# Kernel tuning notes

Hardware: AMD Instinct MI355X
Metric: run time of the kernel (lower is better)

Reference implementation:

```python
import jax, jax.numpy as jnp
import numpy as np

B, IN, H, L = 128, 256, 1024, 256
nA, nB = H // 2, (H - 1) // 2        # pairs per A-layer / B-layer
LB = L // 2
LA = L - LB                           # A layers come first when L is odd
PI = float(np.pi)


def setup_inputs() -> dict:
    key = jax.random.key(0)
    ks = jax.random.split(key, 14)
    u = lambda k, shp: jax.random.uniform(k, shp, minval=-PI, maxval=PI)
    return {
        "inputsR": jax.random.normal(ks[0], (B, IN), dtype=jnp.float32),
        "inputsI": jax.random.normal(ks[1], (B, IN), dtype=jnp.float32),
        "stateR": jax.random.normal(ks[2], (B, H), dtype=jnp.float32),
        "stateI": jax.random.normal(ks[3], (B, H), dtype=jnp.float32),
        # CLinear params (init_scale=0.01 inside RNNCellCmplx)
        "weightR": 0.01 * jax.random.normal(ks[4], (H, IN), dtype=jnp.float32),
        "weightI": 0.01 * jax.random.normal(ks[5], (H, IN), dtype=jnp.float32),
        "biasR": 0.01 * jax.random.normal(ks[6], (H,), dtype=jnp.float32),
        "biasI": 0.01 * jax.random.normal(ks[7], (H,), dtype=jnp.float32),
        # Clements mesh angles, uniform(-pi, pi)
        "angleA0": u(ks[8], (LA, nA)),
        "angleA1": u(ks[9], (LA, nA)),
        "angleB0": u(ks[10], (LB, nB)),
        "angleB1": u(ks[11], (LB, nB)),
        # diagonal phase + modReLU bias (both init to zero)
        "omega": jnp.zeros((H,), dtype=jnp.float32),
        "mod_bias": jnp.zeros((H,), dtype=jnp.float32),
    }


def _mzi(ar, ai, br, bi, th0, th1):
    """PSDC MZI on channel pairs: phase shifter e^{i*th0} on arm a, then a
    directional coupler with coupling angle th1 (unitary 2x2)."""
    c0, s0 = jnp.cos(th0), jnp.sin(th0)
    pr = c0 * ar - s0 * ai          # p = e^{i th0} * a
    pi_ = s0 * ar + c0 * ai
    c, s = jnp.cos(th1), jnp.sin(th1)
    oar = c * pr - s * bi           # a' = cos*p + i sin*b
    oai = c * pi_ + s * br
    obr = c * br - s * pi_          # b' = i sin*p + cos*b
    obi = c * bi + s * pr
    return oar, oai, obr, obi


def _layerA(xr, xi, t0, t1):
    Bs, N = xr.shape
    oar, oai, obr, obi = _mzi(xr[:, 0::2], xi[:, 0::2], xr[:, 1::2], xi[:, 1::2], t0, t1)
    xr = jnp.stack([oar, obr], axis=-1).reshape(Bs, N)
    xi = jnp.stack([oai, obi], axis=-1).reshape(Bs, N)
    return xr, xi


def _layerB(xr, xi, t0, t1):
    Bs, N = xr.shape  # pairs (1,2),(3,4),... ; channels 0 and N-1 pass through
    oar, oai, obr, obi = _mzi(xr[:, 1:-1:2], xi[:, 1:-1:2], xr[:, 2::2], xi[:, 2::2], t0, t1)
    midr = jnp.stack([oar, obr], axis=-1).reshape(Bs, N - 2)
    midi = jnp.stack([oai, obi], axis=-1).reshape(Bs, N - 2)
    xr = jnp.concatenate([xr[:, :1], midr, xr[:, -1:]], axis=1)
    xi = jnp.concatenate([xi[:, :1], midi, xi[:, -1:]], axis=1)
    return xr, xi


def _clements(xr, xi, A0, A1, B0, B1):
    def step(carry, ang):
        cr, ci = carry
        a0, a1, b0, b1 = ang
        cr, ci = _layerA(cr, ci, a0, a1)
        cr, ci = _layerB(cr, ci, b0, b1)
        return (cr, ci), None
    (xr, xi), _ = jax.lax.scan(step, (xr, xi), (A0[:LB], A1[:LB], B0, B1))
    for k in range(LB, LA):  # trailing A layer when num_layers is odd (static)
        xr, xi = _layerA(xr, xi, A0[k], A1[k])
    return xr, xi


def _forward(inputsR, inputsI, stateR, stateI, weightR, weightI, biasR, biasI,
             angleA0, angleA1, angleB0, angleB1, omega, mod_bias):
    # CLinear: complex y = W x + b
    ihR = inputsR @ weightR.T - inputsI @ weightI.T + biasR
    ihI = inputsR @ weightI.T + inputsI @ weightR.T + biasI
    # Clements unitary mesh on hidden state
    hr, hi = _clements(stateR, stateI, angleA0, angleA1, angleB0, angleB1)
    # diagonal phase e^{i omega}
    co, so = jnp.cos(omega), jnp.sin(omega)
    hhR = co * hr - so * hi
    hhI = so * hr + co * hi
    # complex add
    zr = ihR + hhR
    zi = ihI + hhI
    # modReLU: relu(|z| + b) * z / |z|
    mag = jnp.sqrt(zr * zr + zi * zi)
    scale = jax.nn.relu(mag + mod_bias) / jnp.maximum(mag, 1e-8)
    return jnp.stack([scale * zr, scale * zi])  # (2, B, H)


def reference(inputsR, inputsI, stateR, stateI, weightR, weightI, biasR, biasI,
              angleA0, angleA1, angleB0, angleB1, omega, mod_bias):
    return _forward(inputsR, inputsI, stateR, stateI, weightR, weightI, biasR, biasI,
                    angleA0, angleA1, angleB0, angleB1, omega, mod_bias)
```

## Files before the change

### kernel.cpp

```cpp
#include <hip/hip_runtime.h>
#include <math.h>

#define NBATCH 128
#define NIN    256
#define NH     1024
#define NSTEPS 128
#define NA     512
#define NB     511
#define NBP    512

#define TABA_OFF 0
#define TABB_OFF (NSTEPS * NBP * 4)
#define IHR_OFF  (TABB_OFF + NSTEPS * NBP * 4)
#define IHI_OFF  (IHR_OFF + NBATCH * NH)

__global__ __launch_bounds__(256) void trig_kernel(
    const float* __restrict__ A0, const float* __restrict__ A1,
    const float* __restrict__ B0, const float* __restrict__ B1,
    float* __restrict__ ws)
{
    int idx = blockIdx.x * blockDim.x + threadIdx.x;
    const int totalA = NSTEPS * NA;
    const int totalB = NSTEPS * NB;
    if (idx < totalA) {
        int l = idx >> 9;
        int p = idx & 511;
        float a0 = A0[idx], a1 = A1[idx];
        float4 v = make_float4(cosf(a0), sinf(a0), cosf(a1), sinf(a1));
        ((float4*)(ws + TABA_OFF))[l * NBP + p] = v;
    } else {
        int j = idx - totalA;
        if (j < totalB) {
            int l = j / NB;
            int p = j - l * NB;
            float b0 = B0[j], b1 = B1[j];
            float4 v = make_float4(cosf(b0), sinf(b0), cosf(b1), sinf(b1));
            ((float4*)(ws + TABB_OFF))[l * NBP + p] = v;
        }
    }
}

__global__ __launch_bounds__(256) void gemm_kernel(
    const float* __restrict__ inR, const float* __restrict__ inI,
    const float* __restrict__ wR,  const float* __restrict__ wI,
    const float* __restrict__ biasR, const float* __restrict__ biasI,
    float* __restrict__ ws)
{
    __shared__ float ldsR[16 * 260];
    __shared__ float ldsI[16 * 260];
    const int h0 = blockIdx.x * 16;
    const int b0 = blockIdx.y * 16;
    const int tid = threadIdx.x;

    for (int e = tid; e < 16 * 64; e += 256) {
        int bb = e >> 6;
        int k4 = e & 63;
        float4 vr = ((const float4*)(inR + (b0 + bb) * NIN))[k4];
        float4 vi = ((const float4*)(inI + (b0 + bb) * NIN))[k4];
        *(float4*)&ldsR[bb * 260 + k4 * 4] = vr;
        *(float4*)&ldsI[bb * 260 + k4 * 4] = vi;
    }
    __syncthreads();

    const int hl = tid & 15, bl = tid >> 4;
    const int h = h0 + hl, bb = b0 + bl;
    const float4* wr4 = (const float4*)(wR + h * NIN);
    const float4* wi4 = (const float4*)(wI + h * NIN);

    float accR = 0.f, accI = 0.f;
#pragma unroll 8
    for (int k4 = 0; k4 < 64; ++k4) {
        float4 wr = wr4[k4];
        float4 wi = wi4[k4];
        float4 xr = *(const float4*)&ldsR[bl * 260 + k4 * 4];
        float4 xi = *(const float4*)&ldsI[bl * 260 + k4 * 4];
        accR += xr.x * wr.x - xi.x * wi.x;
        accI += xr.x * wi.x + xi.x * wr.x;
        accR += xr.y * wr.y - xi.y * wi.y;
        accI += xr.y * wi.y + xi.y * wr.y;
        accR += xr.z * wr.z - xi.z * wi.z;
        accI += xr.z * wi.z + xi.z * wr.z;
        accR += xr.w * wr.w - xi.w * wi.w;
        accI += xr.w * wi.w + xi.w * wr.w;
    }
    float* ihR = ws + IHR_OFF;
    float* ihI = ws + IHI_OFF;
    ihR[bb * NH + h] = accR + biasR[h];
    ihI[bb * NH + h] = accI + biasI[h];
}

__global__ __launch_bounds__(256) void mesh_kernel(
    const float* __restrict__ stateR, const float* __restrict__ stateI,
    const float* __restrict__ omega,  const float* __restrict__ mod_bias,
    const float* __restrict__ ws, float* __restrict__ out)
{
    __shared__ float xch[2][2][256][2];

    const int b = blockIdx.x;
    const int t = threadIdx.x;
    const float4* tA = (const float4*)(ws + TABA_OFF);
    const float4* tB = (const float4*)(ws + TABB_OFF);

    float4 sr = ((const float4*)(stateR + b * NH))[t];
    float4 si = ((const float4*)(stateI + b * NH))[t];
    float cr0 = sr.x, cr1 = sr.y, cr2 = sr.z, cr3 = sr.w;
    float ci0 = si.x, ci1 = si.y, ci2 = si.z, ci3 = si.w;

    float4 a0  = tA[2 * t];
    float4 a1  = tA[2 * t + 1];
    float4 b_l = tB[2 * t - 1];
    float4 b_c = tB[2 * t];
    float4 b_r = tB[2 * t + 1];

    for (int l = 0; l < NSTEPS; ++l) {
        const int ln = (l < NSTEPS - 1) ? (l + 1) : (NSTEPS - 1);
        float4 na0 = tA[ln * NBP + 2 * t];
        float4 na1 = tA[ln * NBP + 2 * t + 1];
        float4 nbl = tB[ln * NBP + 2 * t - 1];
        float4 nbc = tB[ln * NBP + 2 * t];
        float4 nbr = tB[ln * NBP + 2 * t + 1];

        {
            float pr = a0.x * cr0 - a0.y * ci0;
            float pi = a0.y * cr0 + a0.x * ci0;
            float tr = cr1, ti = ci1;
            cr0 = a0.z * pr - a0.w * ti;
            ci0 = a0.z * pi + a0.w * tr;
            cr1 = a0.z * tr - a0.w * pi;
            ci1 = a0.z * ti + a0.w * pr;
        }
        {
            float pr = a1.x * cr2 - a1.y * ci2;
            float pi = a1.y * cr2 + a1.x * ci2;
            float tr = cr3, ti = ci3;
            cr2 = a1.z * pr - a1.w * ti;
            ci2 = a1.z * pi + a1.w * tr;
            cr3 = a1.z * tr - a1.w * pi;
            ci3 = a1.z * ti + a1.w * pr;
        }

        const int buf = l & 1;
        xch[buf][0][t][0] = cr0; xch[buf][0][t][1] = ci0;
        xch[buf][1][t][0] = cr3; xch[buf][1][t][1] = ci3;
        __syncthreads();

        {
            float pr = b_c.x * cr1 - b_c.y * ci1;
            float pi = b_c.y * cr1 + b_c.x * ci1;
            float tr = cr2, ti = ci2;
            cr1 = b_c.z * pr - b_c.w * ti;
            ci1 = b_c.z * pi + b_c.w * tr;
            cr2 = b_c.z * tr - b_c.w * pi;
            ci2 = b_c.z * ti + b_c.w * pr;
        }
        if (t < 255) {
            float rr = xch[buf][0][t + 1][0];
            float ri = xch[buf][0][t + 1][1];
            float pr = b_r.x * cr3 - b_r.y * ci3;
            float pi = b_r.y * cr3 + b_r.x * ci3;
            cr3 = b_r.z * pr - b_r.w * ri;
            ci3 = b_r.z * pi + b_r.w * rr;
        }
        if (t > 0) {
            float lr = xch[buf][1][t - 1][0];
            float li = xch[buf][1][t - 1][1];
            float pr = b_l.x * lr - b_l.y * li;
            float pi = b_l.y * lr + b_l.x * li;
            float nr = b_l.z * cr0 - b_l.w * pi;
            float ni = b_l.z * ci0 + b_l.w * pr;
            cr0 = nr; ci0 = ni;
        }

        a0 = na0; a1 = na1; b_l = nbl; b_c = nbc; b_r = nbr;
    }

    float4 om = ((const float4*)omega)[t];
    float4 mb = ((const float4*)mod_bias)[t];
    float4 ir = ((const float4*)(ws + IHR_OFF + b * NH))[t];
    float4 ii = ((const float4*)(ws + IHI_OFF + b * NH))[t];

    float hr[4] = {cr0, cr1, cr2, cr3};
    float hi[4] = {ci0, ci1, ci2, ci3};
    float oms[4] = {om.x, om.y, om.z, om.w};
    float mbs[4] = {mb.x, mb.y, mb.z, mb.w};
    float irs[4] = {ir.x, ir.y, ir.z, ir.w};
    float iis[4] = {ii.x, ii.y, ii.z, ii.w};
    float orr[4], ori[4];
#pragma unroll
    for (int j = 0; j < 4; ++j) {
        float co = cosf(oms[j]);
        float so = sinf(oms[j]);
        float hhR = co * hr[j] - so * hi[j];
        float hhI = so * hr[j] + co * hi[j];
        float zr = irs[j] + hhR;
        float zi = iis[j] + hhI;
        float mag = sqrtf(zr * zr + zi * zi);
        float sc = fmaxf(mag + mbs[j], 0.f) / fmaxf(mag, 1e-8f);
        orr[j] = sc * zr;
        ori[j] = sc * zi;
    }
    float4 o0 = make_float4(orr[0], orr[1], orr[2], orr[3]);
    float4 o1 = make_float4(ori[0], ori[1], ori[2], ori[3]);
    ((float4*)(out + b * NH))[t] = o0;
    ((float4*)(out + NBATCH * NH + b * NH))[t] = o1;
}

extern "C" void kernel_launch(void* const* d_in, const int* in_sizes, int n_in,
                              void* d_out, int out_size, void* d_ws, size_t ws_size,
                              hipStream_t stream)
{
    const float* inputsR = (const float*)d_in[0];
    const float* inputsI = (const float*)d_in[1];
    const float* stateR  = (const float*)d_in[2];
    const float* stateI  = (const float*)d_in[3];
    const float* weightR = (const float*)d_in[4];
    const float* weightI = (const float*)d_in[5];
    const float* biasR   = (const float*)d_in[6];
    const float* biasI   = (const float*)d_in[7];
    const float* angleA0 = (const float*)d_in[8];
    const float* angleA1 = (const float*)d_in[9];
    const float* angleB0 = (const float*)d_in[10];
    const float* angleB1 = (const float*)d_in[11];
    const float* omega   = (const float*)d_in[12];
    const float* mod_b   = (const float*)d_in[13];
    float* ws = (float*)d_ws;
    float* out = (float*)d_out;

    {
        int total = NSTEPS * NA + NSTEPS * NB;
        int blocks = (total + 255) / 256;
        hipLaunchKernelGGL(trig_kernel, dim3(blocks), dim3(256), 0, stream,
                           angleA0, angleA1, angleB0, angleB1, ws);
    }
    hipLaunchKernelGGL(gemm_kernel, dim3(NH / 16, NBATCH / 16), dim3(256), 0,
                       stream, inputsR, inputsI, weightR, weightI,
                       biasR, biasI, ws);
    hipLaunchKernelGGL(mesh_kernel, dim3(NBATCH), dim3(256), 0, stream,
                       stateR, stateI, omega, mod_b, ws, out);
}
```

Before: 165.6 us.

## Run mesh in one wavefront per batch row with shuffles, merge prep kernels

The mesh kernel now uses a single 64-lane wavefront per batch row, with each lane holding 16 channels in registers. Neighbour exchange across lanes goes through wave shuffles, which removes the shared-memory exchange and the per-layer block barrier. The trig tables are re-laid out as lane-interleaved so each lane's loads coalesce, and the complex GEMM is retiled with LDS staging and merged with the trig precompute into one launch. Only 128 wavefronts run the serial mesh, so GPU occupancy is very low, and each lane does four times the arithmetic plus register pressure from prefetching 17 float4 values.

```diff
diff --git a/kernel.cpp b/kernel.cpp
--- a/kernel.cpp
+++ b/kernel.cpp
@@ -7,202 +7,229 @@
 #define NSTEPS 128
 #define NA     512
 #define NB     511
-#define NBP    512
 
 #define TABA_OFF 0
-#define TABB_OFF (NSTEPS * NBP * 4)
-#define IHR_OFF  (TABB_OFF + NSTEPS * NBP * 4)
+#define TABB_OFF (NSTEPS * 512 * 4)
+#define IHR_OFF  (TABB_OFF + NSTEPS * 512 * 4)
 #define IHI_OFF  (IHR_OFF + NBATCH * NH)
 
-__global__ __launch_bounds__(256) void trig_kernel(
+#define GEMM_BLOCKS 128
+#define PREP_BLOCKS (GEMM_BLOCKS + 512)
+
+__global__ __launch_bounds__(256) void prep_kernel(
+    const float* __restrict__ inR, const float* __restrict__ inI,
+    const float* __restrict__ wR,  const float* __restrict__ wI,
+    const float* __restrict__ biasR, const float* __restrict__ biasI,
     const float* __restrict__ A0, const float* __restrict__ A1,
     const float* __restrict__ B0, const float* __restrict__ B1,
     float* __restrict__ ws)
 {
-    int idx = blockIdx.x * blockDim.x + threadIdx.x;
-    const int totalA = NSTEPS * NA;
-    const int totalB = NSTEPS * NB;
-    if (idx < totalA) {
-        int l = idx >> 9;
-        int p = idx & 511;
-        float a0 = A0[idx], a1 = A1[idx];
-        float4 v = make_float4(cosf(a0), sinf(a0), cosf(a1), sinf(a1));
-        ((float4*)(ws + TABA_OFF))[l * NBP + p] = v;
-    } else {
-        int j = idx - totalA;
-        if (j < totalB) {
-            int l = j / NB;
-            int p = j - l * NB;
-            float b0 = B0[j], b1 = B1[j];
-            float4 v = make_float4(cosf(b0), sinf(b0), cosf(b1), sinf(b1));
-            ((float4*)(ws + TABB_OFF))[l * NBP + p] = v;
-        }
+    __shared__ float xr_s[64][68], xi_s[64][68];
+    __shared__ float wr_s[16][68], wi_s[16][68];
+
+    if (blockIdx.x >= GEMM_BLOCKS) {
+        int idx = (blockIdx.x - GEMM_BLOCKS) * 256 + threadIdx.x;
+        const int totalA = NSTEPS * NA;
+        const int totalB = NSTEPS * NB;
+        float4* tA = (float4*)(ws + TABA_OFF);
+        float4* tB = (float4*)(ws + TABB_OFF);
+        if (idx < totalA) {
+            int l = idx >> 9, p = idx & 511;
+            int lane = p >> 3, j = p & 7;
+            float a0 = A0[idx], a1 = A1[idx];
+            tA[l * 512 + j * 64 + lane] =
+                make_float4(cosf(a0), sinf(a0), cosf(a1), sinf(a1));
+        } else if (idx < totalA + totalB) {
+            int q = idx - totalA;
+            int l = q / NB, p = q - l * NB;
+            int lane = p >> 3, j = p & 7;
+            float b0 = B0[q], b1 = B1[q];
+            tB[l * 512 + j * 64 + lane] =
+                make_float4(cosf(b0), sinf(b0), cosf(b1), sinf(b1));
+        } else {
+            int l = idx - (totalA + totalB);
+            tB[l * 512 + 511] = make_float4(1.f, 0.f, 1.f, 0.f);
+        }
+        return;
+    }
+
+    const int bid = blockIdx.x;
+    const int h0 = (bid >> 1) * 16;
+    const int b0 = (bid & 1) * 64;
+    const int tid = threadIdx.x;
+    const int hl = tid & 15, bg = tid >> 4;
+
+    float accR[4] = {0.f, 0.f, 0.f, 0.f};
+    float accI[4] = {0.f, 0.f, 0.f, 0.f};
+
+    for (int kt = 0; kt < 4; ++kt) {
+        const int k0 = kt * 64;
+        __syncthreads();
+        {
+            int row = tid >> 4, col = tid & 15;
+#pragma unroll
+            for (int pass = 0; pass < 4; ++pass) {
+                int r = pass * 16 + row;
+                float4 vr = *(const float4*)(inR + (b0 + r) * NIN + k0 + col * 4);
+                float4 vi = *(const float4*)(inI + (b0 + r) * NIN + k0 + col * 4);
+                *(float4*)&xr_s[r][col * 4] = vr;
+                *(float4*)&xi_s[r][col * 4] = vi;
+            }
+            float4 vr = *(const float4*)(wR + (h0 + row) * NIN + k0 + col * 4);
+            float4 vi = *(const float4*)(wI + (h0 + row) * NIN + k0 + col * 4);
+            *(float4*)&wr_s[row][col * 4] = vr;
+            *(float4*)&wi_s[row][col * 4] = vi;
+        }
+        __syncthreads();
+#pragma unroll 4
+        for (int k4 = 0; k4 < 16; ++k4) {
+            float4 wr = *(const float4*)&wr_s[hl][k4 * 4];
+            float4 wi = *(const float4*)&wi_s[hl][k4 * 4];
+#pragma unroll
+            for (int j = 0; j < 4; ++j) {
+                int bl = bg * 4 + j;
+                float4 xr = *(const float4*)&xr_s[bl][k4 * 4];
+                float4 xi = *(const float4*)&xi_s[bl][k4 * 4];
+                accR[j] += xr.x * wr.x - xi.x * wi.x
+                         + xr.y * wr.y - xi.y * wi.y
+                         + xr.z * wr.z - xi.z * wi.z
+                         + xr.w * wr.w - xi.w * wi.w;
+                accI[j] += xr.x * wi.x + xi.x * wr.x
+                         + xr.y * wi.y + xi.y * wr.y
+                         + xr.z * wi.z + xi.z * wr.z
+                         + xr.w * wi.w + xi.w * wr.w;
+            }
+        }
+    }
+    const float br = biasR[h0 + hl], bi = biasI[h0 + hl];
+#pragma unroll
+    for (int j = 0; j < 4; ++j) {
+        int b = b0 + bg * 4 + j;
+        ws[IHR_OFF + b * NH + h0 + hl] = accR[j] + br;
+        ws[IHI_OFF + b * NH + h0 + hl] = accI[j] + bi;
     }
 }
 
-__global__ __launch_bounds__(256) void gemm_kernel(
-    const float* __restrict__ inR, const float* __restrict__ inI,
-    const float* __restrict__ wR,  const float* __restrict__ wI,
-    const float* __restrict__ biasR, const float* __restrict__ biasI,
-    float* __restrict__ ws)
-{
-    __shared__ float ldsR[16 * 260];
-    __shared__ float ldsI[16 * 260];
-    const int h0 = blockIdx.x * 16;
-    const int b0 = blockIdx.y * 16;
-    const int tid = threadIdx.x;
-
-    for (int e = tid; e < 16 * 64; e += 256) {
-        int bb = e >> 6;
-        int k4 = e & 63;
-        float4 vr = ((const float4*)(inR + (b0 + bb) * NIN))[k4];
-        float4 vi = ((const float4*)(inI + (b0 + bb) * NIN))[k4];
-        *(float4*)&ldsR[bb * 260 + k4 * 4] = vr;
-        *(float4*)&ldsI[bb * 260 + k4 * 4] = vi;
-    }
-    __syncthreads();
-
-    const int hl = tid & 15, bl = tid >> 4;
-    const int h = h0 + hl, bb = b0 + bl;
-    const float4* wr4 = (const float4*)(wR + h * NIN);
-    const float4* wi4 = (const float4*)(wI + h * NIN);
-
-    float accR = 0.f, accI = 0.f;
-#pragma unroll 8
-    for (int k4 = 0; k4 < 64; ++k4) {
-        float4 wr = wr4[k4];
-        float4 wi = wi4[k4];
-        float4 xr = *(const float4*)&ldsR[bl * 260 + k4 * 4];
-        float4 xi = *(const float4*)&ldsI[bl * 260 + k4 * 4];
-        accR += xr.x * wr.x - xi.x * wi.x;
-        accI += xr.x * wi.x + xi.x * wr.x;
-        accR += xr.y * wr.y - xi.y * wi.y;
-        accI += xr.y * wi.y + xi.y * wr.y;
-        accR += xr.z * wr.z - xi.z * wi.z;
-        accI += xr.z * wi.z + xi.z * wr.z;
-        accR += xr.w * wr.w - xi.w * wi.w;
-        accI += xr.w * wi.w + xi.w * wr.w;
-    }
-    float* ihR = ws + IHR_OFF;
-    float* ihI = ws + IHI_OFF;
-    ihR[bb * NH + h] = accR + biasR[h];
-    ihI[bb * NH + h] = accI + biasI[h];
-}
-
-__global__ __launch_bounds__(256) void mesh_kernel(
+__global__ __launch_bounds__(64) void mesh_kernel(
     const float* __restrict__ stateR, const float* __restrict__ stateI,
     const float* __restrict__ omega,  const float* __restrict__ mod_bias,
     const float* __restrict__ ws, float* __restrict__ out)
 {
-    __shared__ float xch[2][2][256][2];
-
     const int b = blockIdx.x;
-    const int t = threadIdx.x;
+    const int lane = threadIdx.x;
     const float4* tA = (const float4*)(ws + TABA_OFF);
     const float4* tB = (const float4*)(ws + TABB_OFF);
 
-    float4 sr = ((const float4*)(stateR + b * NH))[t];
-    float4 si = ((const float4*)(stateI + b * NH))[t];
-    float cr0 = sr.x, cr1 = sr.y, cr2 = sr.z, cr3 = sr.w;
-    float ci0 = si.x, ci1 = si.y, ci2 = si.z, ci3 = si.w;
-
-    float4 a0  = tA[2 * t];
-    float4 a1  = tA[2 * t + 1];
-    float4 b_l = tB[2 * t - 1];
-    float4 b_c = tB[2 * t];
-    float4 b_r = tB[2 * t + 1];
+    float cr[16], ci[16];
+    {
+        const float4* sr4 = (const float4*)(stateR + b * NH + lane * 16);
+        const float4* si4 = (const float4*)(stateI + b * NH + lane * 16);
+#pragma unroll
+        for (int q = 0; q < 4; ++q) {
+            float4 r = sr4[q], i = si4[q];
+            cr[4 * q] = r.x; cr[4 * q + 1] = r.y; cr[4 * q + 2] = r.z; cr[4 * q + 3] = r.w;
+            ci[4 * q] = i.x; ci[4 * q + 1] = i.y; ci[4 * q + 2] = i.z; ci[4 * q + 3] = i.w;
+        }
+    }
+
+    const int blIdx = (lane == 0) ? 511 : (447 + lane);
+
+    float4 A[8], Bv[8], BL;
+#pragma unroll
+    for (int j = 0; j < 8; ++j) {
+        A[j]  = tA[j * 64 + lane];
+        Bv[j] = tB[j * 64 + lane];
+    }
+    BL = tB[blIdx];
 
     for (int l = 0; l < NSTEPS; ++l) {
-        const int ln = (l < NSTEPS - 1) ? (l + 1) : (NSTEPS - 1);
-        float4 na0 = tA[ln * NBP + 2 * t];
-        float4 na1 = tA[ln * NBP + 2 * t + 1];
-        float4 nbl = tB[ln * NBP + 2 * t - 1];
-        float4 nbc = tB[ln * NBP + 2 * t];
-        float4 nbr = tB[ln * NBP + 2 * t + 1];
-
+        const int ln = (l < NSTEPS - 1) ? l + 1 : l;
+        const int baseN = ln * 512;
+        float4 nA[8], nB_[8], nBL;
+#pragma unroll
+        for (int j = 0; j < 8; ++j) {
+            nA[j]  = tA[baseN + j * 64 + lane];
+            nB_[j] = tB[baseN + j * 64 + lane];
+        }
+        nBL = tB[baseN + blIdx];
+
+#pragma unroll
+        for (int j = 0; j < 8; ++j) {
+            float ar = cr[2 * j], ai = ci[2 * j];
+            float br = cr[2 * j + 1], bi = ci[2 * j + 1];
+            float pr = A[j].x * ar - A[j].y * ai;
+            float pi = A[j].y * ar + A[j].x * ai;
+            cr[2 * j]     = A[j].z * pr - A[j].w * bi;
+            ci[2 * j]     = A[j].z * pi + A[j].w * br;
+            cr[2 * j + 1] = A[j].z * br - A[j].w * pi;
+            ci[2 * j + 1] = A[j].z * bi + A[j].w * pr;
+        }
+
+        float rc0r  = __shfl_down(cr[0], 1, 64);
+        float rc0i  = __shfl_down(ci[0], 1, 64);
+        float lc15r = __shfl_up(cr[15], 1, 64);
+        float lc15i = __shfl_up(ci[15], 1, 64);
+
+#pragma unroll
+        for (int j = 0; j < 7; ++j) {
+            float ar = cr[2 * j + 1], ai = ci[2 * j + 1];
+            float br = cr[2 * j + 2], bi = ci[2 * j + 2];
+            float pr = Bv[j].x * ar - Bv[j].y * ai;
+            float pi = Bv[j].y * ar + Bv[j].x * ai;
+            cr[2 * j + 1] = Bv[j].z * pr - Bv[j].w * bi;
+            ci[2 * j + 1] = Bv[j].z * pi + Bv[j].w * br;
+            cr[2 * j + 2] = Bv[j].z * br - Bv[j].w * pi;
+            ci[2 * j + 2] = Bv[j].z * bi + Bv[j].w * pr;
+        }
         {
-            float pr = a0.x * cr0 - a0.y * ci0;
-            float pi = a0.y * cr0 + a0.x * ci0;
-            float tr = cr1, ti = ci1;
-            cr0 = a0.z * pr - a0.w * ti;
-            ci0 = a0.z * pi + a0.w * tr;
-            cr1 = a0.z * tr - a0.w * pi;
-            ci1 = a0.z * ti + a0.w * pr;
+            float pr = Bv[7].x * cr[15] - Bv[7].y * ci[15];
+            float pi = Bv[7].y * cr[15] + Bv[7].x * ci[15];
+            cr[15] = Bv[7].z * pr - Bv[7].w * rc0i;
+            ci[15] = Bv[7].z * pi + Bv[7].w * rc0r;
         }
         {
-            float pr = a1.x * cr2 - a1.y * ci2;
-            float pi = a1.y * cr2 + a1.x * ci2;
-            float tr = cr3, ti = ci3;
-            cr2 = a1.z * pr - a1.w * ti;
-            ci2 = a1.z * pi + a1.w * tr;
-            cr3 = a1.z * tr - a1.w * pi;
-            ci3 = a1.z * ti + a1.w * pr;
-        }
-
-        const int buf = l & 1;
-        xch[buf][0][t][0] = cr0; xch[buf][0][t][1] = ci0;
-        xch[buf][1][t][0] = cr3; xch[buf][1][t][1] = ci3;
-        __syncthreads();
-
-        {
-            float pr = b_c.x * cr1 - b_c.y * ci1;
-            float pi = b_c.y * cr1 + b_c.x * ci1;
-            float tr = cr2, ti = ci2;
-            cr1 = b_c.z * pr - b_c.w * ti;
-            ci1 = b_c.z * pi + b_c.w * tr;
-            cr2 = b_c.z * tr - b_c.w * pi;
-            ci2 = b_c.z * ti + b_c.w * pr;
-        }
-        if (t < 255) {
-            float rr = xch[buf][0][t + 1][0];
-            float ri = xch[buf][0][t + 1][1];
-            float pr = b_r.x * cr3 - b_r.y * ci3;
-            float pi = b_r.y * cr3 + b_r.x * ci3;
-            cr3 = b_r.z * pr - b_r.w * ri;
-            ci3 = b_r.z * pi + b_r.w * rr;
-        }
-        if (t > 0) {
-            float lr = xch[buf][1][t - 1][0];
-            float li = xch[buf][1][t - 1][1];
-            float pr = b_l.x * lr - b_l.y * li;
-            float pi = b_l.y * lr + b_l.x * li;
-            float nr = b_l.z * cr0 - b_l.w * pi;
-            float ni = b_l.z * ci0 + b_l.w * pr;
-            cr0 = nr; ci0 = ni;
-        }
-
-        a0 = na0; a1 = na1; b_l = nbl; b_c = nbc; b_r = nbr;
-    }
-
-    float4 om = ((const float4*)omega)[t];
-    float4 mb = ((const float4*)mod_bias)[t];
-    float4 ir = ((const float4*)(ws + IHR_OFF + b * NH))[t];
-    float4 ii = ((const float4*)(ws + IHI_OFF + b * NH))[t];
-
-    float hr[4] = {cr0, cr1, cr2, cr3};
-    float hi[4] = {ci0, ci1, ci2, ci3};
-    float oms[4] = {om.x, om.y, om.z, om.w};
-    float mbs[4] = {mb.x, mb.y, mb.z, mb.w};
-    float irs[4] = {ir.x, ir.y, ir.z, ir.w};
-    float iis[4] = {ii.x, ii.y, ii.z, ii.w};
-    float orr[4], ori[4];
-#pragma unroll
-    for (int j = 0; j < 4; ++j) {
-        float co = cosf(oms[j]);
-        float so = sinf(oms[j]);
-        float hhR = co * hr[j] - so * hi[j];
-        float hhI = so * hr[j] + co * hi[j];
-        float zr = irs[j] + hhR;
-        float zi = iis[j] + hhI;
-        float mag = sqrtf(zr * zr + zi * zi);
-        float sc = fmaxf(mag + mbs[j], 0.f) / fmaxf(mag, 1e-8f);
-        orr[j] = sc * zr;
-        ori[j] = sc * zi;
-    }
-    float4 o0 = make_float4(orr[0], orr[1], orr[2], orr[3]);
-    float4 o1 = make_float4(ori[0], ori[1], ori[2], ori[3]);
-    ((float4*)(out + b * NH))[t] = o0;
-    ((float4*)(out + NBATCH * NH + b * NH))[t] = o1;
+            float pr = BL.x * lc15r - BL.y * lc15i;
+            float pi = BL.y * lc15r + BL.x * lc15i;
+            float nr = BL.z * cr[0] - BL.w * pi;
+            float ni = BL.z * ci[0] + BL.w * pr;
+            cr[0] = nr; ci[0] = ni;
+        }
+
+#pragma unroll
+        for (int j = 0; j < 8; ++j) { A[j] = nA[j]; Bv[j] = nB_[j]; }
+        BL = nBL;
+    }
+
+    const float4* ir4 = (const float4*)(ws + IHR_OFF + b * NH + lane * 16);
+    const float4* ii4 = (const float4*)(ws + IHI_OFF + b * NH + lane * 16);
+    const float4* om4 = (const float4*)(omega + lane * 16);
+    const float4* mb4 = (const float4*)(mod_bias + lane * 16);
+    float4* o0p = (float4*)(out + b * NH + lane * 16);
+    float4* o1p = (float4*)(out + NBATCH * NH + b * NH + lane * 16);
+#pragma unroll
+    for (int q = 0; q < 4; ++q) {
+        float4 ir = ir4[q], ii = ii4[q], om = om4[q], mb = mb4[q];
+        float irs[4] = {ir.x, ir.y, ir.z, ir.w};
+        float iis[4] = {ii.x, ii.y, ii.z, ii.w};
+        float oms[4] = {om.x, om.y, om.z, om.w};
+        float mbs[4] = {mb.x, mb.y, mb.z, mb.w};
+        float o0[4], o1[4];
+#pragma unroll
+        for (int jj = 0; jj < 4; ++jj) {
+            int j = q * 4 + jj;
+            float co = cosf(oms[jj]), so = sinf(oms[jj]);
+            float hhR = co * cr[j] - so * ci[j];
+            float hhI = so * cr[j] + co * ci[j];
+            float zr = irs[jj] + hhR;
+            float zi = iis[jj] + hhI;
+            float mag = sqrtf(zr * zr + zi * zi);
+            float sc = fmaxf(mag + mbs[jj], 0.f) / fmaxf(mag, 1e-8f);
+            o0[jj] = sc * zr;
+            o1[jj] = sc * zi;
+        }
+        o0p[q] = make_float4(o0[0], o0[1], o0[2], o0[3]);
+        o1p[q] = make_float4(o1[0], o1[1], o1[2], o1[3]);
+    }
 }
 
 extern "C" void kernel_launch(void* const* d_in, const int* in_sizes, int n_in,
@@ -226,15 +253,9 @@
     float* ws = (float*)d_ws;
     float* out = (float*)d_out;
 
-    {
-        int total = NSTEPS * NA + NSTEPS * NB;
-        int blocks = (total + 255) / 256;
-        hipLaunchKernelGGL(trig_kernel, dim3(blocks), dim3(256), 0, stream,
-                           angleA0, angleA1, angleB0, angleB1, ws);
-    }
-    hipLaunchKernelGGL(gemm_kernel, dim3(NH / 16, NBATCH / 16), dim3(256), 0,
-                       stream, inputsR, inputsI, weightR, weightI,
-                       biasR, biasI, ws);
-    hipLaunchKernelGGL(mesh_kernel, dim3(NBATCH), dim3(256), 0, stream,
+    hipLaunchKernelGGL(prep_kernel, dim3(PREP_BLOCKS), dim3(256), 0, stream,
+                       inputsR, inputsI, weightR, weightI, biasR, biasI,
+                       angleA0, angleA1, angleB0, angleB1, ws);
+    hipLaunchKernelGGL(mesh_kernel, dim3(NBATCH), dim3(64), 0, stream,
                        stateR, stateI, omega, mod_b, ws, out);
 }
```

Measured after the change: 206.8 us. +24.9%, slower.
